# Kernel optimization log

Measured on AMD Instinct MI355X. Metric: run time of the kernel, lower is better.

## Reference

```python
import jax, jax.numpy as jnp
import numpy as np

K = 2
ALPHA = 1.0
EPS = 1e-6


def _bce_logits(x, z):
    # binary_cross_entropy_with_logits, elementwise, numerically stable
    return jax.nn.softplus(x) - x * z


def _unfold(x, i):
    # F.unfold(x, kernel_size=2i+1, padding=i) for x: [B,1,H,W] -> [B, P, H*W]
    ks = 2 * i + 1
    p = jax.lax.conv_general_dilated_patches(
        x, (ks, ks), (1, 1), [(i, i), (i, i)])  # [B, ks*ks, H, W], zero-padded
    B = x.shape[0]
    return p.reshape(B, ks * ks, -1)


def setup_inputs() -> dict:
    key = jax.random.key(0)
    k1, k2 = jax.random.split(key)
    B, H, W = 8, 512, 512
    pred = jax.random.normal(k1, (B, 1, H, W), dtype=jnp.float32)
    target = jax.random.randint(k2, (B, 1, H, W), 0, 2).astype(jnp.float32)
    return {"pred": pred, "target": target}


def reference(pred, target):
    B, _, H, W = pred.shape
    N = H * W
    bce = _bce_logits(pred, target).reshape(B, 1, N)  # [B,1,N]
    total = jnp.zeros((B, N), dtype=pred.dtype)
    for i in range(1, K + 1):
        ks = 2 * i + 1
        P = ks * ks
        c = P // 2
        up = _unfold(pred, i)                      # [B,P,N]
        ut = _unfold(target, i)                    # [B,P,N]
        vm = _unfold(jnp.ones_like(target), i) == 0  # True where padding
        cp = up[:, c:c + 1, :]                     # center logits [B,1,N]
        ct = ut[:, c:c + 1, :]
        joint = cp * up
        lab = ct * ut
        mutual = _bce_logits(joint, lab)
        pairwise = jnp.exp(-jax.nn.sigmoid(cp) * jax.nn.sigmoid(up))
        loss = bce / (mutual + ALPHA * pairwise + EPS)
        loss = jnp.where(vm, jnp.asarray(1.0, loss.dtype), loss)
        total = total + (0.5 ** (i - 1)) * (loss.sum(axis=1) / P)
    return total.mean()
```

## Files before the change

kernel.cpp:

```cpp
#include <hip/hip_runtime.h>

#define TILE 32
#define HALO 2
#define LH (TILE + HALO)
#define LW (TILE + 2 * HALO)
#define EPS 1e-6f


constexpr float W_IN  = 1.0f / 9.0f + 0.02f;
constexpr float W_OUT = 0.02f;

__device__ __forceinline__ float log1p_poly(float u) {
    const float w = (u - 0.5f) * 0.6666666667f;
    float s = 0.14285714f;
    s = __builtin_fmaf(s, w, -0.16666667f);
    s = __builtin_fmaf(s, w, 0.20f);
    s = __builtin_fmaf(s, w, -0.25f);
    s = __builtin_fmaf(s, w, 0.33333333f);
    s = __builtin_fmaf(s, w, -0.50f);
    s = __builtin_fmaf(s, w, 1.0f);
    return __builtin_fmaf(s, w, 0.40546511f);
}

__device__ __forceinline__ float expneg01_poly(float x) {
    const float z = x - 0.5f;
    float s = -0.0083333333f;
    s = __builtin_fmaf(s, z, 0.041666667f);
    s = __builtin_fmaf(s, z, -0.16666667f);
    s = __builtin_fmaf(s, z, 0.5f);
    s = __builtin_fmaf(s, z, -1.0f);
    s = __builtin_fmaf(s, z, 1.0f);
    return s * 0.60653066f;
}

__device__ __forceinline__ void pair_nd(const float4 ca, const float4 cb, float w,
                                        float& n, float& d) {
    const float j   = ca.x * cb.x;
    const float lab = ca.y * cb.y;
    const float u   = __expf(-fabsf(j));
    const float sp  = fmaxf(j, 0.f) + log1p_poly(u);
    const float m   = sp - j * lab;
    const float pw  = expneg01_poly(ca.z * cb.z);
    const float dd  = m + pw + EPS;
    const float nn  = w * (ca.w + cb.w);
    const bool oob  = cb.z < 0.f;
    n = oob ? w : nn;
    d = oob ? 1.f : dd;
}

__global__ __launch_bounds__(256) void scloss_main(
    const float* __restrict__ pred, const float* __restrict__ target,
    float* __restrict__ out, int B, int H, int W, double inv_cnt) {
    __shared__ float4 sh[LH * LW];

    const int tilesX = W / TILE;
    const int tilesPer = tilesX * (H / TILE);
    const int b = blockIdx.x / tilesPer;
    const int tile = blockIdx.x % tilesPer;
    const int ty0 = (tile / tilesX) * TILE;
    const int tx0 = (tile % tilesX) * TILE;

    const float* pbase = pred + (size_t)b * H * W;
    const float* tbase = target + (size_t)b * H * W;
    const int tid = threadIdx.x;

    for (int idx = tid; idx < LH * LW; idx += 256) {
        const int cy = idx / LW, cx = idx % LW;
        const int gy = ty0 + cy;
        const int gx = tx0 + cx - HALO;
        float p = 0.f, t = 0.f, g = -1.f, bce = 0.f;
        if (gy < H && gx >= 0 && gx < W) {
            p = pbase[gy * W + gx];
            t = tbase[gy * W + gx];
            g = __builtin_amdgcn_rcpf(1.f + __expf(-p));
            bce = fmaxf(p, 0.f) + log1p_poly(__expf(-fabsf(p))) - p * t;
        }
        sh[idx] = make_float4(p, t, g, bce);
    }
    __syncthreads();

    const int px = tid & 31;
    const int py0 = tid >> 5;
    float acc = 0.f;

    const bool negCheck = (ty0 == 0) || (tx0 == 0) || (tx0 + TILE == W);

    constexpr int pdy[12] = {0, 0, 1, 1, 1, 1, 1, 2, 2, 2, 2, 2};
    constexpr int pdx[12] = {1, 2, -2, -1, 0, 1, 2, -2, -1, 0, 1, 2};
    constexpr float pw12[12] = {W_IN, W_OUT, W_OUT, W_IN, W_IN, W_IN,
                                W_OUT, W_OUT, W_OUT, W_OUT, W_OUT, W_OUT};

    #pragma unroll
    for (int r = 0; r < 4; ++r) {
        const int ay = py0 + r * 8;
        const float4* base = &sh[ay * LW + px + HALO];
        const float4 ca = base[0];

        {
            float n, d;
            pair_nd(ca, ca, W_IN * 0.5f, n, d);
            acc += n * __builtin_amdgcn_rcpf(d);
        }

        #pragma unroll
        for (int k = 0; k < 12; k += 2) {
            float n1, d1, n2, d2;
            pair_nd(ca, base[pdy[k] * LW + pdx[k]], pw12[k], n1, d1);
            pair_nd(ca, base[pdy[k + 1] * LW + pdx[k + 1]], pw12[k + 1], n2, d2);
            const float num = n1 * d2 + n2 * d1;
            acc += num * __builtin_amdgcn_rcpf(d1 * d2);
        }

        if (negCheck) {
            const int gy = ty0 + ay, gx = tx0 + px;
            #pragma unroll
            for (int k = 0; k < 12; ++k) {
                const int ny = gy - pdy[k], nx = gx - pdx[k];
                if (ny < 0 || nx < 0 || nx >= W) acc += pw12[k];
            }
        }
    }

    #pragma unroll
    for (int off = 32; off > 0; off >>= 1)
        acc += __shfl_down(acc, off, 64);
    __shared__ double wsum[4];
    if ((tid & 63) == 0) wsum[tid >> 6] = (double)acc;
    __syncthreads();
    if (tid == 0) {
        const double s = wsum[0] + wsum[1] + wsum[2] + wsum[3];
        atomicAdd(out, (float)(s * inv_cnt));
    }
}

extern "C" void kernel_launch(void* const* d_in, const int* in_sizes, int n_in,
                              void* d_out, int out_size, void* d_ws, size_t ws_size,
                              hipStream_t stream) {
    const float* pred   = (const float*)d_in[0];
    const float* target = (const float*)d_in[1];
    float* out = (float*)d_out;

    const int H = 512, W = 512;
    const int B = in_sizes[0] / (H * W);
    const int nblocks = B * (H / TILE) * (W / TILE);

    hipMemsetAsync(out, 0, sizeof(float), stream);
    scloss_main<<<nblocks, 256, 0, stream>>>(pred, target, out, B, H, W,
                                             1.0 / ((double)B * H * W));
}
```

Baseline: 101.9 us.

## Vectorize pair math, combine all fractions into one reciprocal, correct borders analytically

The pair loss is now computed two neighbours at a time using packed float2 math, and the log1p/exp polynomials are shortened. All 13 numerator/denominator pairs per pixel are merged into one fraction so each pixel needs a single reciprocal instead of seven. Out-of-bounds neighbours are no longer flagged in shared memory; they are treated as zero-padded values and then fixed by an explicit edge correction using a precomputed constant. Shorter polynomials and a product of 13 denominators could lose accuracy or overflow when denominators are large.

```diff
diff --git a/kernel.cpp b/kernel.cpp
--- a/kernel.cpp
+++ b/kernel.cpp
@@ -4,48 +4,43 @@
 #define HALO 2
 #define LH (TILE + HALO)
 #define LW (TILE + 2 * HALO)
-#define EPS 1e-6f
 
+typedef float v2f __attribute__((ext_vector_type(2)));
 
 constexpr float W_IN  = 1.0f / 9.0f + 0.02f;
 constexpr float W_OUT = 0.02f;
+constexpr float INV_D_OOB = 0.59090266f;
 
-__device__ __forceinline__ float log1p_poly(float u) {
-    const float w = (u - 0.5f) * 0.6666666667f;
-    float s = 0.14285714f;
-    s = __builtin_fmaf(s, w, -0.16666667f);
-    s = __builtin_fmaf(s, w, 0.20f);
-    s = __builtin_fmaf(s, w, -0.25f);
-    s = __builtin_fmaf(s, w, 0.33333333f);
-    s = __builtin_fmaf(s, w, -0.50f);
-    s = __builtin_fmaf(s, w, 1.0f);
-    return __builtin_fmaf(s, w, 0.40546511f);
-}
+__device__ __forceinline__ v2f vsp(float x) { v2f r; r.x = x; r.y = x; return r; }
 
-__device__ __forceinline__ float expneg01_poly(float x) {
-    const float z = x - 0.5f;
-    float s = -0.0083333333f;
-    s = __builtin_fmaf(s, z, 0.041666667f);
-    s = __builtin_fmaf(s, z, -0.16666667f);
-    s = __builtin_fmaf(s, z, 0.5f);
-    s = __builtin_fmaf(s, z, -1.0f);
-    s = __builtin_fmaf(s, z, 1.0f);
-    return s * 0.60653066f;
-}
+__device__ __forceinline__ void pair2(const float4 ca, const float4 cb1, const float4 cb2,
+                                      float w1, float w2, float& N, float& D) {
+    v2f qx; qx.x = cb1.x; qx.y = cb2.x;
+    v2f qy; qy.x = cb1.y; qy.y = cb2.y;
+    v2f qz; qz.x = cb1.z; qz.y = cb2.z;
+    v2f qw; qw.x = cb1.w; qw.y = cb2.w;
 
-__device__ __forceinline__ void pair_nd(const float4 ca, const float4 cb, float w,
-                                        float& n, float& d) {
-    const float j   = ca.x * cb.x;
-    const float lab = ca.y * cb.y;
-    const float u   = __expf(-fabsf(j));
-    const float sp  = fmaxf(j, 0.f) + log1p_poly(u);
-    const float m   = sp - j * lab;
-    const float pw  = expneg01_poly(ca.z * cb.z);
-    const float dd  = m + pw + EPS;
-    const float nn  = w * (ca.w + cb.w);
-    const bool oob  = cb.z < 0.f;
-    n = oob ? w : nn;
-    d = oob ? 1.f : dd;
+    const v2f j = qx * vsp(ca.x);
+    v2f u;
+    u.x = __expf(-fabsf(j.x));
+    u.y = __expf(-fabsf(j.y));
+    const v2f t = (u - vsp(0.5f)) * vsp(0.66666667f);
+    v2f s = __builtin_elementwise_fma(t, vsp(-0.25f), vsp(0.33333333f));
+    s = __builtin_elementwise_fma(s, t, vsp(-0.5f));
+    s = __builtin_elementwise_fma(s, t, vsp(1.0f));
+    v2f sp = __builtin_elementwise_fma(s, t, vsp(0.40546511f));
+    sp = sp + __builtin_elementwise_max(j, vsp(0.0f));
+    const v2f m = sp - j * (qy * vsp(ca.y));
+    const v2f z = qz * vsp(ca.z) - vsp(0.5f);
+    v2f e = __builtin_elementwise_fma(z, vsp(0.041666667f), vsp(-0.16666667f));
+    e = __builtin_elementwise_fma(e, z, vsp(0.5f));
+    e = __builtin_elementwise_fma(e, z, vsp(-1.0f));
+    e = __builtin_elementwise_fma(e, z, vsp(1.0f));
+    const v2f d = __builtin_elementwise_fma(e, vsp(0.60653066f), m + vsp(1e-6f));
+    v2f wv; wv.x = w1; wv.y = w2;
+    const v2f n = (qw + vsp(ca.w)) * wv;
+    N = n.x * d.y + n.y * d.x;
+    D = d.x * d.y;
 }
 
 __global__ __launch_bounds__(256) void scloss_main(
@@ -68,12 +63,18 @@
         const int cy = idx / LW, cx = idx % LW;
         const int gy = ty0 + cy;
         const int gx = tx0 + cx - HALO;
-        float p = 0.f, t = 0.f, g = -1.f, bce = 0.f;
+        float p = 0.f, t = 0.f, g = 0.f, bce = 0.f;
         if (gy < H && gx >= 0 && gx < W) {
             p = pbase[gy * W + gx];
             t = tbase[gy * W + gx];
-            g = __builtin_amdgcn_rcpf(1.f + __expf(-p));
-            bce = fmaxf(p, 0.f) + log1p_poly(__expf(-fabsf(p))) - p * t;
+            const float en = __expf(-fabsf(p));
+            const float inv = __builtin_amdgcn_rcpf(1.f + en);
+            g = (p >= 0.f) ? inv : en * inv;
+            const float tt = (en - 0.5f) * 0.66666667f;
+            float ss = fmaf(tt, -0.25f, 0.33333333f);
+            ss = fmaf(ss, tt, -0.5f);
+            ss = fmaf(ss, tt, 1.0f);
+            bce = fmaf(ss, tt, 0.40546511f) + fmaxf(p, 0.f) - p * t;
         }
         sh[idx] = make_float4(p, t, g, bce);
     }
@@ -83,7 +84,7 @@
     const int py0 = tid >> 5;
     float acc = 0.f;
 
-    const bool negCheck = (ty0 == 0) || (tx0 == 0) || (tx0 + TILE == W);
+    const bool edge = (tx0 == 0) | (tx0 + TILE == W) | (ty0 == 0) | (ty0 + TILE == H);
 
     constexpr int pdy[12] = {0, 0, 1, 1, 1, 1, 1, 2, 2, 2, 2, 2};
     constexpr int pdx[12] = {1, 2, -2, -1, 0, 1, 2, -2, -1, 0, 1, 2};
@@ -96,27 +97,46 @@
         const float4* base = &sh[ay * LW + px + HALO];
         const float4 ca = base[0];
 
-        {
-            float n, d;
-            pair_nd(ca, ca, W_IN * 0.5f, n, d);
-            acc += n * __builtin_amdgcn_rcpf(d);
-        }
+        const float j0 = ca.x * ca.x;
+        const float u0 = __expf(-j0);
+        const float t0 = (u0 - 0.5f) * 0.66666667f;
+        float s0 = fmaf(t0, -0.25f, 0.33333333f);
+        s0 = fmaf(s0, t0, -0.5f);
+        s0 = fmaf(s0, t0, 1.0f);
+        const float sp0 = fmaf(s0, t0, 0.40546511f) + j0;
+        const float m0 = sp0 - j0 * (ca.y * ca.y);
+        const float z0 = ca.z * ca.z - 0.5f;
+        float e0 = fmaf(z0, 0.041666667f, -0.16666667f);
+        e0 = fmaf(e0, z0, 0.5f);
+        e0 = fmaf(e0, z0, -1.0f);
+        e0 = fmaf(e0, z0, 1.0f);
+        const float d0 = fmaf(e0, 0.60653066f, m0 + 1e-6f);
+        const float n0 = W_IN * ca.w;
 
-        #pragma unroll
-        for (int k = 0; k < 12; k += 2) {
-            float n1, d1, n2, d2;
-            pair_nd(ca, base[pdy[k] * LW + pdx[k]], pw12[k], n1, d1);
-            pair_nd(ca, base[pdy[k + 1] * LW + pdx[k + 1]], pw12[k + 1], n2, d2);
-            const float num = n1 * d2 + n2 * d1;
-            acc += num * __builtin_amdgcn_rcpf(d1 * d2);
-        }
+        float N1, D1, N2, D2, N3, D3, N4, D4, N5, D5, N6, D6;
+        pair2(ca, base[1],          base[2],          W_IN,  W_OUT, N1, D1);
+        pair2(ca, base[LW - 2],     base[LW - 1],     W_OUT, W_IN,  N2, D2);
+        pair2(ca, base[LW],         base[LW + 1],     W_IN,  W_IN,  N3, D3);
+        pair2(ca, base[LW + 2],     base[2 * LW - 2], W_OUT, W_OUT, N4, D4);
+        pair2(ca, base[2 * LW - 1], base[2 * LW],     W_OUT, W_OUT, N5, D5);
+        pair2(ca, base[2 * LW + 1], base[2 * LW + 2], W_OUT, W_OUT, N6, D6);
 
-        if (negCheck) {
+        const float Na = n0 * D1 + N1 * d0, Da = d0 * D1;
+        const float Nb = N2 * D3 + N3 * D2, Db = D2 * D3;
+        const float Nc = N4 * D5 + N5 * D4, Dc = D4 * D5;
+        const float Nd = Na * Db + Nb * Da, Dd = Da * Db;
+        const float Ne = Nc * D6 + N6 * Dc, De = Dc * D6;
+        const float Nf = Nd * De + Ne * Dd, Df = Dd * De;
+        acc += Nf * __builtin_amdgcn_rcpf(Df);
+
+        if (edge) {
             const int gy = ty0 + ay, gx = tx0 + px;
             #pragma unroll
             for (int k = 0; k < 12; ++k) {
-                const int ny = gy - pdy[k], nx = gx - pdx[k];
-                if (ny < 0 || nx < 0 || nx >= W) acc += pw12[k];
+                if (gy + pdy[k] >= H || gx + pdx[k] < 0 || gx + pdx[k] >= W)
+                    acc += pw12[k] * (1.f - ca.w * INV_D_OOB);
+                if (gy - pdy[k] < 0 || gx - pdx[k] < 0 || gx - pdx[k] >= W)
+                    acc += pw12[k];
             }
         }
     }
```

New measurement: 98.50 us. 1.03x faster.
